# Performance work log

Hardware: AMD Instinct MI355X
Metric: run time of the kernel (lower is better)

The kernel has to match this reference:

```python
import jax, jax.numpy as jnp
import numpy as np

N, E, B = 25600, 307200, 256
H, D, F0, K = 256, 16, 7, 6
GNN_OUT, TDA_IN, TDA_OUT, MEG_IN, MEG_OUT = 192, 32, 128, 16, 64
FUSION = GNN_OUT + TDA_OUT + MEG_OUT  # 384
MID = FUSION // 2  # 192


def _ln(x, g, b, eps=1e-5):
    m = x.mean(-1, keepdims=True)
    v = x.var(-1, keepdims=True)
    return (x - m) * jax.lax.rsqrt(v + eps) * g + b


def _ntn(x, pos, neg):
    return jnp.nan_to_num(x, nan=0.0, posinf=pos, neginf=neg)


def setup_inputs():
    key = jax.random.key(0)
    ks = iter(jax.random.split(key, 80))
    p = lambda *s: 0.05 * jax.random.normal(next(ks), s, jnp.float32)
    inp = {
        "x": jax.random.normal(next(ks), (N, F0), jnp.float32),
        "edge_attr": jax.random.uniform(next(ks), (E, D), dtype=jnp.float32),
        "tda": jax.random.normal(next(ks), (B, TDA_IN), jnp.float32),
        "megnet": jax.random.normal(next(ks), (B, MEG_IN), jnp.float32),
        "edge_index": jax.random.randint(next(ks), (2, E), 0, N),
        "batch": jnp.repeat(jnp.arange(B), N // B),
        # GNN encoder
        "gin_W": p(F0, H), "gin_b": jnp.zeros(H),
        "conv_Wf": p(6, 2 * H + D, H), "conv_bf": jnp.zeros((6, H)),
        "conv_Ws": p(6, 2 * H + D, H), "conv_bs": jnp.zeros((6, H)),
        "gln_g": jnp.ones((6, H)), "gln_b": jnp.zeros((6, H)),
        "gout_W": p(H, GNN_OUT), "gout_b": jnp.zeros(GNN_OUT),
        # TDA projector 32->256->256->128
        "t1_W": p(TDA_IN, 2 * TDA_OUT), "t1_b": jnp.zeros(2 * TDA_OUT),
        "tln1_g": jnp.ones(2 * TDA_OUT), "tln1_b": jnp.zeros(2 * TDA_OUT),
        "t2_W": p(2 * TDA_OUT, 2 * TDA_OUT), "t2_b": jnp.zeros(2 * TDA_OUT),
        "tln2_g": jnp.ones(2 * TDA_OUT), "tln2_b": jnp.zeros(2 * TDA_OUT),
        "t3_W": p(2 * TDA_OUT, TDA_OUT), "t3_b": jnp.zeros(TDA_OUT),
        # MEGNet projector 16->128->128->64
        "m1_W": p(MEG_IN, 2 * MEG_OUT), "m1_b": jnp.zeros(2 * MEG_OUT),
        "mln1_g": jnp.ones(2 * MEG_OUT), "mln1_b": jnp.zeros(2 * MEG_OUT),
        "m2_W": p(2 * MEG_OUT, 2 * MEG_OUT), "m2_b": jnp.zeros(2 * MEG_OUT),
        "mln2_g": jnp.ones(2 * MEG_OUT), "mln2_b": jnp.zeros(2 * MEG_OUT),
        "m3_W": p(2 * MEG_OUT, MEG_OUT), "m3_b": jnp.zeros(MEG_OUT),
        # fusion LN
        "fln_g": jnp.ones(FUSION), "fln_b": jnp.zeros(FUSION),
        # CPPN gate 384->48->24->6
        "g1_W": p(FUSION, K * 8), "g1_b": jnp.zeros(K * 8),
        "hln_g": jnp.ones(K * 8), "hln_b": jnp.zeros(K * 8),
        "g2_W": p(K * 8, K * 4), "g2_b": jnp.zeros(K * 4),
        "g3_W": p(K * 4, K), "g3_b": jnp.zeros(K),
        # CPPN poly branches stacked over K
        "plin_W": p(K, FUSION), "plin_b": jnp.zeros(K),
        "pq1_W": p(K, FUSION, MID), "pq1_b": jnp.zeros((K, MID)),
        "pq2_W": p(K, MID), "pq2_b": jnp.zeros(K),
        "pc1_W": p(K, FUSION, MID // 2), "pc1_b": jnp.zeros((K, MID // 2)),
        "pc2_W": p(K, MID // 2), "pc2_b": jnp.zeros(K),
    }
    return inp


def _forward(x, edge_attr, tda, megnet, edge_index, batch,
             gin_W, gin_b, conv_Wf, conv_bf, conv_Ws, conv_bs, gln_g, gln_b, gout_W, gout_b,
             t1_W, t1_b, tln1_g, tln1_b, t2_W, t2_b, tln2_g, tln2_b, t3_W, t3_b,
             m1_W, m1_b, mln1_g, mln1_b, m2_W, m2_b, mln2_g, mln2_b, m3_W, m3_b,
             fln_g, fln_b,
             g1_W, g1_b, hln_g, hln_b, g2_W, g2_b, g3_W, g3_b,
             plin_W, plin_b, pq1_W, pq1_b, pq2_W, pq2_b, pc1_W, pc1_b, pc2_W, pc2_b):
    silu = jax.nn.silu
    tda = _ntn(tda, 3.0, -3.0)
    megnet = _ntn(megnet, 3.0, -3.0)
    x = _ntn(x, 3.0, -3.0)
    ea = _ntn(edge_attr, 1.0, 0.0)
    src, dst = edge_index[0], edge_index[1]

    h = silu(x @ gin_W + gin_b)  # [N, H]
    for i in range(6):
        # CGConv message: z_ij = [x_i, x_j, e_ij]; sigmoid(z Wf) * softplus(z Ws); sum-agg + root
        z = jnp.concatenate([h[dst], h[src], ea], axis=-1)  # [E, 2H+D]
        msg = jax.nn.sigmoid(z @ conv_Wf[i] + conv_bf[i]) * jax.nn.softplus(z @ conv_Ws[i] + conv_bs[i])
        conv = h + jax.ops.segment_sum(msg, dst, num_segments=N)
        h = _ln(silu(conv) + h, gln_g[i], gln_b[i])
    cnt = jax.ops.segment_sum(jnp.ones((N, 1), h.dtype), batch, num_segments=B)
    pooled = jax.ops.segment_sum(h, batch, num_segments=B) / jnp.maximum(cnt, 1.0)
    z_gnn = jnp.nan_to_num(pooled @ gout_W + gout_b)  # [B, 192]

    # --- projectors ---
    a = _ln(silu(tda @ t1_W + t1_b), tln1_g, tln1_b)
    a = _ln(silu(a @ t2_W + t2_b), tln2_g, tln2_b)
    z_tda = jnp.nan_to_num(a @ t3_W + t3_b)  # [B, 128]
    m = _ln(silu(megnet @ m1_W + m1_b), mln1_g, mln1_b)
    m = _ln(silu(m @ m2_W + m2_b), mln2_g, mln2_b)
    z_meg = jnp.nan_to_num(m @ m3_W + m3_b)  # [B, 64]

    z = _ln(jnp.concatenate([z_gnn, z_tda, z_meg], axis=-1), fln_g, fln_b)  # [B, 384]

    # --- CPPN mixture head ---
    g = _ln(silu(z @ g1_W + g1_b), hln_g, hln_b)
    g = silu(g @ g2_W + g2_b)
    gates = jax.nn.softmax(g @ g3_W + g3_b, axis=-1)  # [B, K]
    lin = jnp.einsum('bd,kd->bk', z, plin_W) + plin_b
    hq = silu(jnp.einsum('bd,kdm->bkm', z, pq1_W) + pq1_b)  # [B, K, 192]
    q = jnp.einsum('bkm,km->bk', hq, pq2_W) + pq2_b
    hc = silu(jnp.einsum('bd,kdm->bkm', z, pc1_W) + pc1_b) ** 2  # [B, K, 96]
    c = jnp.einsum('bkm,km->bk', hc, pc2_W) + pc2_b
    y = (gates * (lin + q + c)).sum(-1)  # [B]
    return y, z


def reference(x, edge_attr, tda, megnet, edge_index, batch,
              gin_W, gin_b, conv_Wf, conv_bf, conv_Ws, conv_bs, gln_g, gln_b, gout_W, gout_b,
              t1_W, t1_b, tln1_g, tln1_b, t2_W, t2_b, tln2_g, tln2_b, t3_W, t3_b,
              m1_W, m1_b, mln1_g, mln1_b, m2_W, m2_b, mln2_g, mln2_b, m3_W, m3_b,
              fln_g, fln_b,
              g1_W, g1_b, hln_g, hln_b, g2_W, g2_b, g3_W, g3_b,
              plin_W, plin_b, pq1_W, pq1_b, pq2_W, pq2_b, pc1_W, pc1_b, pc2_W, pc2_b):
    return _forward(x, edge_attr, tda, megnet, edge_index, batch,
                    gin_W, gin_b, conv_Wf, conv_bf, conv_Ws, conv_bs, gln_g, gln_b, gout_W, gout_b,
                    t1_W, t1_b, tln1_g, tln1_b, t2_W, t2_b, tln2_g, tln2_b, t3_W, t3_b,
                    m1_W, m1_b, mln1_g, mln1_b, m2_W, m2_b, mln2_g, mln2_b, m3_W, m3_b,
                    fln_g, fln_b,
                    g1_W, g1_b, hln_g, hln_b, g2_W, g2_b, g3_W, g3_b,
                    plin_W, plin_b, pq1_W, pq1_b, pq2_W, pq2_b, pc1_W, pc1_b, pc2_W, pc2_b)
```

## Files before the change

### kernel.cpp

```cpp
#include <hip/hip_runtime.h>
#include <hip/hip_bf16.h>
#include <cmath>

#define NN 25600
#define NE 307200
#define NB 256
#define HD 256

typedef __attribute__((ext_vector_type(8))) short short8;
typedef __attribute__((ext_vector_type(4))) float f32x4;
typedef __attribute__((ext_vector_type(2))) float f32x2;
typedef __attribute__((ext_vector_type(2))) _Float16 h16x2;
typedef __attribute__((ext_vector_type(2))) __fp16 fp16x2;

__device__ __forceinline__ float ntn_f(float v, float pos, float neg) {
  if (isnan(v)) return 0.f;
  if (isinf(v)) return v > 0.f ? pos : neg;
  return v;
}
__device__ __forceinline__ float ntn_def(float v) {
  if (isnan(v)) return 0.f;
  if (isinf(v)) return v > 0.f ? 3.4028234663852886e38f : -3.4028234663852886e38f;
  return v;
}
__device__ __forceinline__ float sigmoid_f(float x) { return 1.f / (1.f + __expf(-x)); }
__device__ __forceinline__ float silu_f(float x) { return x * sigmoid_f(x); }
__device__ __forceinline__ float softplus_f(float x) {
  return fmaxf(x, 0.f) + __logf(1.f + __expf(-fabsf(x)));
}
__device__ __forceinline__ unsigned short f2bf(float f) {
  unsigned int u = __float_as_uint(f);
  u += 0x7fffu + ((u >> 16) & 1u);
  return (unsigned short)(u >> 16);
}
__device__ __forceinline__ float bfu(unsigned short u) {
  return __uint_as_float((unsigned int)u << 16);
}
__device__ __forceinline__ h16x2 u2h(unsigned int u) {
  union { unsigned int u; h16x2 h; } x; x.u = u; return x.h;
}
__device__ __forceinline__ unsigned int pk2u(float a, float b) {
  union { fp16x2 p; unsigned int u; } x;
  x.p = __builtin_amdgcn_cvt_pkrtz(a, b);
  return x.u;
}
#if __has_builtin(__builtin_amdgcn_fdot2)
#define FDOT2(a, b, c) __builtin_amdgcn_fdot2((a), (b), (c), false)
#else
__device__ __forceinline__ float fdot2_sw(h16x2 a, h16x2 b, float c) {
  return (float)a.x * (float)b.x + (float)a.y * (float)b.y + c;
}
#define FDOT2(a, b, c) fdot2_sw((a), (b), (c))
#endif

template <int NW>
__device__ __forceinline__ float blockSum(float v, float* sred) {
  int lane = threadIdx.x & 63, w = threadIdx.x >> 6;
#pragma unroll
  for (int o = 32; o; o >>= 1) v += __shfl_xor(v, o);
  __syncthreads();
  if (lane == 0) sred[w] = v;
  __syncthreads();
  float r = 0.f;
#pragma unroll
  for (int i = 0; i < NW; ++i) r += sred[i];
  return r;
}

__global__ void k_hist(const int* __restrict__ dst, int* __restrict__ counts, int E) {
  int e = blockIdx.x * 256 + threadIdx.x;
  if (e < E) atomicAdd(&counts[dst[e]], 1);
}

__global__ __launch_bounds__(1024) void k_scan(const int* __restrict__ counts,
                                               int* __restrict__ offs, int n) {
  __shared__ int sd[1024];
  __shared__ int run;
  int tid = threadIdx.x;
  if (tid == 0) run = 0;
  __syncthreads();
  for (int base = 0; base < n; base += 1024) {
    int i = base + tid;
    int v = (i < n) ? counts[i] : 0;
    sd[tid] = v;
    __syncthreads();
    int acc = v;
    for (int off = 1; off < 1024; off <<= 1) {
      int t = (tid >= off) ? sd[tid - off] : 0;
      __syncthreads();
      acc += t;
      sd[tid] = acc;
      __syncthreads();
    }
    int r = run;
    if (i < n) offs[i] = r + acc - v;
    __syncthreads();
    if (tid == 1023) run = r + sd[1023];
    __syncthreads();
  }
  if (threadIdx.x == 0) offs[n] = run;
}

__global__ void k_scatter(const int* __restrict__ dst, const int* __restrict__ offs,
                          int* __restrict__ cursor, int* __restrict__ eidx, int E) {
  int e = blockIdx.x * 256 + threadIdx.x;
  if (e < E) {
    int d = dst[e];
    int p = offs[d] + atomicAdd(&cursor[d], 1);
    eidx[p] = e;
  }
}

__global__ void k_srcperm(const int* __restrict__ eidx, const int* __restrict__ srcArr,
                          int* __restrict__ srcs, int E) {
  int i = blockIdx.x * 256 + threadIdx.x;
  if (i < E) srcs[i] = srcArr[eidx[i]];
}

__global__ void k_eapermh(const int* __restrict__ eidx, const float* __restrict__ ea,
                          unsigned int* __restrict__ eah, int E) {
  int gid = blockIdx.x * 256 + threadIdx.x;
  if (gid < E * 8) {
    int ii = gid >> 3, kp = gid & 7;
    int e = eidx[ii];
    float v0 = ea[(size_t)e * 16 + 2 * kp];
    float v1 = ea[(size_t)e * 16 + 2 * kp + 1];
    eah[gid] = pk2u(v0, v1);
  }
}

__global__ void k_pack(const float* __restrict__ conv_Wf, const float* __restrict__ conv_Ws,
                       unsigned short* __restrict__ w4t) {
  int layer = blockIdx.y;
  int gid = blockIdx.x * 256 + threadIdx.x;
  int k = gid & 255;
  int c = gid >> 8;
  int j = c & 255;
  int tbl = c >> 8;
  const float* W = (tbl < 2) ? conv_Wf : conv_Ws;
  int krow = (tbl & 1) ? 256 + k : k;
  float v = W[((size_t)layer * 528 + krow) * 256 + j];
  w4t[((size_t)layer * 1024 + c) * 256 + k] = f2bf(v);
}

__global__ void k_packEd(const float* __restrict__ conv_Wf, const float* __restrict__ conv_Ws,
                         unsigned int* __restrict__ whd) {
  int layer = blockIdx.y;
  int gid = blockIdx.x * 256 + threadIdx.x;
  int d = gid >> 4, pr = gid & 15;
  int g = pr >> 3, kp = pr & 7;
  const float* W = g ? conv_Ws : conv_Wf;
  float v0 = W[((size_t)layer * 528 + 512 + 2 * kp) * 256 + d];
  float v1 = W[((size_t)layer * 528 + 512 + 2 * kp + 1) * 256 + d];
  whd[((size_t)layer * 256 + d) * 16 + pr] = pk2u(v0, v1);
}

__global__ void k_gin(const float* __restrict__ x, const float* __restrict__ W,
                      const float* __restrict__ bias, float* __restrict__ h,
                      unsigned short* __restrict__ hbf) {
  int n = blockIdx.x, j = threadIdx.x;
  float xv[7];
#pragma unroll
  for (int k = 0; k < 7; ++k) xv[k] = ntn_f(x[n * 7 + k], 3.f, -3.f);
  float acc = bias[j];
#pragma unroll
  for (int k = 0; k < 7; ++k) acc += xv[k] * W[k * 256 + j];
  float o = silu_f(acc);
  h[(size_t)n * 256 + j] = o;
  hbf[(size_t)n * 256 + j] = f2bf(o);
}

__global__ __launch_bounds__(256) void k_gemm_bf16(
    const unsigned short* __restrict__ Abf,
    const unsigned short* __restrict__ w4t,
    const float* __restrict__ bf, const float* __restrict__ bs,
    unsigned short* __restrict__ Pout) {
  __shared__ unsigned short As[128 * 56];
  __shared__ unsigned short Bs[128 * 56];
  int tid = threadIdx.x;
  int lane = tid & 63, w = tid >> 6;
  int wr = w >> 1, wc = w & 1;
  int m0 = blockIdx.x * 128, n0 = blockIdx.y * 128;
  int l15 = lane & 15, l4 = lane >> 4;
  f32x4 acc[4][4];
#pragma unroll
  for (int i = 0; i < 4; ++i)
#pragma unroll
    for (int j = 0; j < 4; ++j) acc[i][j] = (f32x4)0.f;
  for (int kt = 0; kt < 8; ++kt) {
    int k0 = kt * 32;
    if (kt) __syncthreads();
#pragma unroll
    for (int c = 0; c < 2; ++c) {
      int chunk = tid + c * 256;
      int row = chunk >> 2, q = chunk & 3;
      *(uint4*)&As[row * 56 + q * 8] =
          *(const uint4*)&Abf[(size_t)(m0 + row) * 256 + k0 + q * 8];
      *(uint4*)&Bs[row * 56 + q * 8] =
          *(const uint4*)&w4t[(size_t)(n0 + row) * 256 + k0 + q * 8];
    }
    __syncthreads();
    short8 a[4], b[4];
#pragma unroll
    for (int f = 0; f < 4; ++f) {
      a[f] = *(const short8*)&As[(wr * 64 + f * 16 + l15) * 56 + l4 * 8];
      b[f] = *(const short8*)&Bs[(wc * 64 + f * 16 + l15) * 56 + l4 * 8];
    }
#pragma unroll
    for (int i = 0; i < 4; ++i)
#pragma unroll
      for (int j = 0; j < 4; ++j)
        acc[i][j] = __builtin_amdgcn_mfma_f32_16x16x32_bf16(a[i], b[j], acc[i][j], 0, 0, 0);
  }
#pragma unroll
  for (int j = 0; j < 4; ++j) {
    int gcol = n0 + wc * 64 + j * 16 + l15;
    float bias = (gcol < 256) ? bf[gcol] : (gcol >= 512 && gcol < 768) ? bs[gcol - 512] : 0.f;
#pragma unroll
    for (int i = 0; i < 4; ++i) {
#pragma unroll
      for (int r = 0; r < 4; ++r) {
        int grow = m0 + wr * 64 + i * 16 + l4 * 4 + r;
        Pout[(size_t)grow * 1024 + gcol] = f2bf(acc[i][j][r] + bias);
      }
    }
  }
}

__global__ __launch_bounds__(256) void k_edge4(
    const float* __restrict__ h, const unsigned short* __restrict__ P,
    const unsigned int* __restrict__ eah,
    const int* __restrict__ srcs, const int* __restrict__ offs,
    const unsigned int* __restrict__ whd,
    const float* __restrict__ lng, const float* __restrict__ lnb,
    float* __restrict__ hout, unsigned short* __restrict__ hbfout) {
  __shared__ float sr1[4], sr2[4];
  int tid = threadIdx.x, lane = tid & 63, w = tid >> 6;
  int n = blockIdx.x;
  int d = w * 64 + lane;

  unsigned int wk[16];
  {
    const uint4* wb = (const uint4*)(whd + (size_t)d * 16);
#pragma unroll
    for (int q = 0; q < 4; ++q) {
      uint4 t = wb[q];
      wk[q * 4 + 0] = t.x; wk[q * 4 + 1] = t.y;
      wk[q * 4 + 2] = t.z; wk[q * 4 + 3] = t.w;
    }
  }
  float lg = lng[d], lb = lnb[d];
  const unsigned short* Pn = P + (size_t)n * 1024;
  float pfd = bfu(Pn[d]);
  float psd = bfu(Pn[512 + d]);
  float hn = h[(size_t)n * 256 + d];
  float acc = 0.f;
  int e0 = __builtin_amdgcn_readfirstlane(offs[n]);
  int e1 = __builtin_amdgcn_readfirstlane(offs[n + 1]);

  for (int ii = e0; ii < e1; ++ii) {
    int s = srcs[ii];
    const unsigned short* Ps = P + (size_t)s * 1024;
    unsigned short uf = Ps[256 + d];
    unsigned short us = Ps[768 + d];
    const uint4* e4 = (const uint4*)(eah + (size_t)ii * 8);
    uint4 ea0 = e4[0], ea1 = e4[1];
    unsigned int ec[8] = {ea0.x, ea0.y, ea0.z, ea0.w, ea1.x, ea1.y, ea1.z, ea1.w};
    float af = pfd, as_ = psd;
#pragma unroll
    for (int kp = 0; kp < 8; ++kp) {
      h16x2 c = u2h(ec[kp]);
      af = FDOT2(u2h(wk[kp]), c, af);
      as_ = FDOT2(u2h(wk[8 + kp]), c, as_);
    }
    af += bfu(uf);
    as_ += bfu(us);
    acc += sigmoid_f(af) * softplus_f(as_);
  }
  float cv = hn + acc;
  float t = silu_f(cv) + hn;
  float s1 = t, s2 = t * t;
#pragma unroll
  for (int o = 32; o; o >>= 1) {
    s1 += __shfl_xor(s1, o);
    s2 += __shfl_xor(s2, o);
  }
  if (lane == 0) { sr1[w] = s1; sr2[w] = s2; }
  __syncthreads();
  float S1 = sr1[0] + sr1[1] + sr1[2] + sr1[3];
  float S2 = sr2[0] + sr2[1] + sr2[2] + sr2[3];
  float mean = S1 * (1.f / 256.f);
  float var = S2 * (1.f / 256.f) - mean * mean;
  float inv = rsqrtf(var + 1e-5f);
  float o0 = (t - mean) * inv * lg + lb;
  hout[(size_t)n * 256 + d] = o0;
  hbfout[(size_t)n * 256 + d] = f2bf(o0);
}

__global__ __launch_bounds__(256) void k_pool2(const float* __restrict__ h,
                                               float* __restrict__ pooled) {
  int b = blockIdx.x, j = threadIdx.x;
  const float* hp = h + (size_t)b * 100 * 256 + j;
  float s = 0.f;
  for (int i = 0; i < 100; ++i) s += hp[(size_t)i * 256];
  pooled[b * 256 + j] = s * 0.01f;
}

__global__ void k_zgnn(const float* __restrict__ pooled,
                       const float* __restrict__ W, const float* __restrict__ bias,
                       float* __restrict__ zf) {
  int b = blockIdx.x, j = threadIdx.x;
  float acc = bias[j];
  for (int k = 0; k < 256; ++k) acc += pooled[b * 256 + k] * W[k * 192 + j];
  zf[b * 384 + j] = ntn_def(acc);
}

__global__ __launch_bounds__(256) void k_tda(const float* __restrict__ tda,
    const float* __restrict__ W1, const float* __restrict__ b1,
    const float* __restrict__ g1, const float* __restrict__ bb1,
    const float* __restrict__ W2, const float* __restrict__ b2,
    const float* __restrict__ g2, const float* __restrict__ bb2,
    const float* __restrict__ W3, const float* __restrict__ b3, float* __restrict__ zf) {
  __shared__ float sin_[32];
  __shared__ float sa[256];
  __shared__ float sred[4];
  int b = blockIdx.x, tid = threadIdx.x;
  if (tid < 32) sin_[tid] = ntn_f(tda[b * 32 + tid], 3.f, -3.f);
  __syncthreads();
  float v = b1[tid];
#pragma unroll
  for (int k = 0; k < 32; ++k) v += sin_[k] * W1[k * 256 + tid];
  v = silu_f(v);
  float s1 = blockSum<4>(v, sred);
  float s2 = blockSum<4>(v * v, sred);
  float mean = s1 * (1.f / 256.f), var = s2 * (1.f / 256.f) - mean * mean;
  float inv = rsqrtf(var + 1e-5f);
  v = (v - mean) * inv * g1[tid] + bb1[tid];
  sa[tid] = v;
  __syncthreads();
  float v2 = b2[tid];
  for (int k = 0; k < 256; ++k) v2 += sa[k] * W2[k * 256 + tid];
  v2 = silu_f(v2);
  s1 = blockSum<4>(v2, sred);
  s2 = blockSum<4>(v2 * v2, sred);
  mean = s1 * (1.f / 256.f); var = s2 * (1.f / 256.f) - mean * mean;
  inv = rsqrtf(var + 1e-5f);
  v2 = (v2 - mean) * inv * g2[tid] + bb2[tid];
  __syncthreads();
  sa[tid] = v2;
  __syncthreads();
  if (tid < 128) {
    float o = b3[tid];
    for (int k = 0; k < 256; ++k) o += sa[k] * W3[k * 128 + tid];
    zf[b * 384 + 192 + tid] = ntn_def(o);
  }
}

__global__ __launch_bounds__(128) void k_meg(const float* __restrict__ mg,
    const float* __restrict__ W1, const float* __restrict__ b1,
    const float* __restrict__ g1, const float* __restrict__ bb1,
    const float* __restrict__ W2, const float* __restrict__ b2,
    const float* __restrict__ g2, const float* __restrict__ bb2,
    const float* __restrict__ W3, const float* __restrict__ b3, float* __restrict__ zf) {
  __shared__ float sin_[16];
  __shared__ float sa[128];
  __shared__ float sred[2];
  int b = blockIdx.x, tid = threadIdx.x;
  if (tid < 16) sin_[tid] = ntn_f(mg[b * 16 + tid], 3.f, -3.f);
  __syncthreads();
  float v = b1[tid];
#pragma unroll
  for (int k = 0; k < 16; ++k) v += sin_[k] * W1[k * 128 + tid];
  v = silu_f(v);
  float s1 = blockSum<2>(v, sred);
  float s2 = blockSum<2>(v * v, sred);
  float mean = s1 * (1.f / 128.f), var = s2 * (1.f / 128.f) - mean * mean;
  float inv = rsqrtf(var + 1e-5f);
  v = (v - mean) * inv * g1[tid] + bb1[tid];
  sa[tid] = v;
  __syncthreads();
  float v2 = b2[tid];
  for (int k = 0; k < 128; ++k) v2 += sa[k] * W2[k * 128 + tid];
  v2 = silu_f(v2);
  s1 = blockSum<2>(v2, sred);
  s2 = blockSum<2>(v2 * v2, sred);
  mean = s1 * (1.f / 128.f); var = s2 * (1.f / 128.f) - mean * mean;
  inv = rsqrtf(var + 1e-5f);
  v2 = (v2 - mean) * inv * g2[tid] + bb2[tid];
  __syncthreads();
  sa[tid] = v2;
  __syncthreads();
  if (tid < 64) {
    float o = b3[tid];
    for (int k = 0; k < 128; ++k) o += sa[k] * W3[k * 64 + tid];
    zf[b * 384 + 320 + tid] = ntn_def(o);
  }
}

__global__ __launch_bounds__(384) void k_cppn(const float* __restrict__ zf,
    const float* __restrict__ flng, const float* __restrict__ flnb,
    const float* __restrict__ g1W, const float* __restrict__ g1b,
    const float* __restrict__ hg, const float* __restrict__ hb,
    const float* __restrict__ g2W, const float* __restrict__ g2b,
    const float* __restrict__ g3W, const float* __restrict__ g3b,
    const float* __restrict__ plW, const float* __restrict__ plb,
    const float* __restrict__ pq1W, const float* __restrict__ pq1b,
    const float* __restrict__ pq2W, const float* __restrict__ pq2b,
    const float* __restrict__ pc1W, const float* __restrict__ pc1b,
    const float* __restrict__ pc2W, const float* __restrict__ pc2b,
    float* __restrict__ zout, float* __restrict__ y) {
  __shared__ float sz[384];
  __shared__ float sred[6];
  __shared__ float sg[48];
  __shared__ float s24[24];
  __shared__ float gates[6];
  __shared__ float lin[6];
  __shared__ float qv[6], cvv[6];
  __shared__ float mn48, iv48;
  __shared__ float prodq[1152];
  __shared__ float prodc[576];
  int b = blockIdx.x, tid = threadIdx.x;
  int lane = tid & 63, wv = tid >> 6;

  float v = zf[(size_t)b * 384 + tid];
  float s1 = blockSum<6>(v, sred);
  float s2 = blockSum<6>(v * v, sred);
  float mean = s1 * (1.f / 384.f), var = s2 * (1.f / 384.f) - mean * mean;
  float inv = rsqrtf(var + 1e-5f);
  float zv = (v - mean) * inv * flng[tid] + flnb[tid];
  sz[tid] = zv;
  zout[(size_t)b * 384 + tid] = zv;
  __syncthreads();

  {
    int j = tid >> 3, p = tid & 7;
    float a = 0.f;
    for (int d = p; d < 384; d += 8) a += sz[d] * g1W[d * 48 + j];
    a += __shfl_xor(a, 1);
    a += __shfl_xor(a, 2);
    a += __shfl_xor(a, 4);
    if (p == 0) sg[j] = silu_f(a + g1b[j]);
  }
  __syncthreads();
  if (tid < 64) {
    float x = (tid < 48) ? sg[tid] : 0.f;
    float t1 = x, t2 = x * x;
#pragma unroll
    for (int o = 32; o; o >>= 1) {
      t1 += __shfl_xor(t1, o);
      t2 += __shfl_xor(t2, o);
    }
    if (tid == 0) {
      mn48 = t1 * (1.f / 48.f);
      float vr = t2 * (1.f / 48.f) - mn48 * mn48;
      iv48 = rsqrtf(vr + 1e-5f);
    }
  }
  __syncthreads();
  if (tid < 48) sg[tid] = (sg[tid] - mn48) * iv48 * hg[tid] + hb[tid];
  __syncthreads();
  {
    int j = tid >> 4, p = tid & 15;
    int d0 = p * 3;
    float a = sg[d0] * g2W[d0 * 24 + j] + sg[d0 + 1] * g2W[(d0 + 1) * 24 + j] +
              sg[d0 + 2] * g2W[(d0 + 2) * 24 + j];
    a += __shfl_xor(a, 1);
    a += __shfl_xor(a, 2);
    a += __shfl_xor(a, 4);
    a += __shfl_xor(a, 8);
    if (p == 0) s24[j] = silu_f(a + g2b[j]);
  }
  __syncthreads();
  if (tid < 6) {
    float a = g3b[tid];
    for (int k = 0; k < 24; ++k) a += s24[k] * g3W[k * 6 + tid];
    gates[tid] = a;
  }
  __syncthreads();
  if (tid == 0) {
    float mx = gates[0];
    for (int i = 1; i < 6; ++i) mx = fmaxf(mx, gates[i]);
    float s = 0.f;
    for (int i = 0; i < 6; ++i) { gates[i] = __expf(gates[i] - mx); s += gates[i]; }
    float rs = 1.f / s;
    for (int i = 0; i < 6; ++i) gates[i] *= rs;
  }
  {
    float p = 0.f;
    for (int d = lane; d < 384; d += 64) p += sz[d] * plW[wv * 384 + d];
#pragma unroll
    for (int o = 32; o; o >>= 1) p += __shfl_xor(p, o);
    if (lane == 0) lin[wv] = p + plb[wv];
  }
  if (tid < 288) {
    int k = tid / 48, m4 = (tid % 48) * 4;
    f32x4 a = (f32x4)0.f;
    const float* Wp = pq1W + (size_t)k * 384 * 192 + m4;
    for (int d = 0; d < 384; ++d) {
      float4 w4 = *(const float4*)(Wp + (size_t)d * 192);
      float zd = sz[d];
      a.x += zd * w4.x; a.y += zd * w4.y; a.z += zd * w4.z; a.w += zd * w4.w;
    }
#pragma unroll
    for (int r = 0; r < 4; ++r) {
      int m = m4 + r;
      prodq[k * 192 + m] = silu_f(a[r] + pq1b[k * 192 + m]) * pq2W[k * 192 + m];
    }
  }
  if (tid < 144) {
    int k = tid / 24, m4 = (tid % 24) * 4;
    f32x4 a = (f32x4)0.f;
    const float* Wp = pc1W + (size_t)k * 384 * 96 + m4;
    for (int d = 0; d < 384; ++d) {
      float4 w4 = *(const float4*)(Wp + (size_t)d * 96);
      float zd = sz[d];
      a.x += zd * w4.x; a.y += zd * w4.y; a.z += zd * w4.z; a.w += zd * w4.w;
    }
#pragma unroll
    for (int r = 0; r < 4; ++r) {
      int m = m4 + r;
      float sl = silu_f(a[r] + pc1b[k * 96 + m]);
      prodc[k * 96 + m] = sl * sl * pc2W[k * 96 + m];
    }
  }
  __syncthreads();
  {
    float s = prodq[wv * 192 + lane] + prodq[wv * 192 + 64 + lane] +
              prodq[wv * 192 + 128 + lane];
#pragma unroll
    for (int o = 32; o; o >>= 1) s += __shfl_xor(s, o);
    if (lane == 0) qv[wv] = s + pq2b[wv];
    float c = prodc[wv * 96 + lane];
    float c2 = (lane < 32) ? prodc[wv * 96 + 64 + lane] : 0.f;
    float sc = c + c2;
#pragma unroll
    for (int o = 32; o; o >>= 1) sc += __shfl_xor(sc, o);
    if (lane == 0) cvv[wv] = sc + pc2b[wv];
  }
  __syncthreads();
  if (tid == 0) {
    float yy = 0.f;
    for (int k = 0; k < 6; ++k) yy += gates[k] * (lin[k] + qv[k] + cvv[k]);
    y[b] = yy;
  }
}

extern "C" void kernel_launch(void* const* d_in, const int* in_sizes, int n_in,
                              void* d_out, int out_size, void* d_ws, size_t ws_size,
                              hipStream_t stream) {
  const float* x         = (const float*)d_in[0];
  const float* edge_attr = (const float*)d_in[1];
  const float* tda       = (const float*)d_in[2];
  const float* megnet    = (const float*)d_in[3];
  const int*   edge_index= (const int*)d_in[4];
  const float* gin_W = (const float*)d_in[6];
  const float* gin_b = (const float*)d_in[7];
  const float* conv_Wf = (const float*)d_in[8];
  const float* conv_bf = (const float*)d_in[9];
  const float* conv_Ws = (const float*)d_in[10];
  const float* conv_bs = (const float*)d_in[11];
  const float* gln_g = (const float*)d_in[12];
  const float* gln_b = (const float*)d_in[13];
  const float* gout_W = (const float*)d_in[14];
  const float* gout_b = (const float*)d_in[15];
  const float* t1_W = (const float*)d_in[16];
  const float* t1_b = (const float*)d_in[17];
  const float* tln1_g = (const float*)d_in[18];
  const float* tln1_b = (const float*)d_in[19];
  const float* t2_W = (const float*)d_in[20];
  const float* t2_b = (const float*)d_in[21];
  const float* tln2_g = (const float*)d_in[22];
  const float* tln2_b = (const float*)d_in[23];
  const float* t3_W = (const float*)d_in[24];
  const float* t3_b = (const float*)d_in[25];
  const float* m1_W = (const float*)d_in[26];
  const float* m1_b = (const float*)d_in[27];
  const float* mln1_g = (const float*)d_in[28];
  const float* mln1_b = (const float*)d_in[29];
  const float* m2_W = (const float*)d_in[30];
  const float* m2_b = (const float*)d_in[31];
  const float* mln2_g = (const float*)d_in[32];
  const float* mln2_b = (const float*)d_in[33];
  const float* m3_W = (const float*)d_in[34];
  const float* m3_b = (const float*)d_in[35];
  const float* fln_g = (const float*)d_in[36];
  const float* fln_b = (const float*)d_in[37];
  const float* g1_W = (const float*)d_in[38];
  const float* g1_b = (const float*)d_in[39];
  const float* hln_g = (const float*)d_in[40];
  const float* hln_b = (const float*)d_in[41];
  const float* g2_W = (const float*)d_in[42];
  const float* g2_b = (const float*)d_in[43];
  const float* g3_W = (const float*)d_in[44];
  const float* g3_b = (const float*)d_in[45];
  const float* plin_W = (const float*)d_in[46];
  const float* plin_b = (const float*)d_in[47];
  const float* pq1_W = (const float*)d_in[48];
  const float* pq1_b = (const float*)d_in[49];
  const float* pq2_W = (const float*)d_in[50];
  const float* pq2_b = (const float*)d_in[51];
  const float* pc1_W = (const float*)d_in[52];
  const float* pc1_b = (const float*)d_in[53];
  const float* pc2_W = (const float*)d_in[54];
  const float* pc2_b = (const float*)d_in[55];

  float* ws = (float*)d_ws;
  float* hA = ws;
  float* hB = hA + (size_t)NN * 256;
  float* pooled = hB + (size_t)NN * 256;
  float* zf = pooled + (size_t)NB * 256;
  unsigned short* hbfA = (unsigned short*)(zf + (size_t)NB * 384);
  unsigned short* hbfB = hbfA + (size_t)NN * 256;
  unsigned short* Pbf = hbfB + (size_t)NN * 256;
  unsigned short* w4t = Pbf + (size_t)NN * 1024;
  unsigned int* whd6 = (unsigned int*)(w4t + (size_t)6 * 1024 * 256);
  unsigned int* eah = whd6 + (size_t)6 * 256 * 16;
  int* counts = (int*)(eah + (size_t)NE * 8);
  int* cursor = counts + NN;
  int* offs = cursor + NN;
  int* eidx = offs + NN + 1;
  int* srcs = eidx + NE;

  const int* srcArr = edge_index;
  const int* dstArr = edge_index + NE;

  hipMemsetAsync(counts, 0, (size_t)2 * NN * sizeof(int), stream);

  k_hist<<<(NE + 255) / 256, 256, 0, stream>>>(dstArr, counts, NE);
  k_scan<<<1, 1024, 0, stream>>>(counts, offs, NN);
  k_scatter<<<(NE + 255) / 256, 256, 0, stream>>>(dstArr, offs, cursor, eidx, NE);
  k_srcperm<<<(NE + 255) / 256, 256, 0, stream>>>(eidx, srcArr, srcs, NE);
  k_eapermh<<<(NE * 8 + 255) / 256, 256, 0, stream>>>(eidx, edge_attr, eah, NE);
  k_pack<<<dim3(1024, 6), 256, 0, stream>>>(conv_Wf, conv_Ws, w4t);
  k_packEd<<<dim3(16, 6), 256, 0, stream>>>(conv_Wf, conv_Ws, whd6);

  k_gin<<<NN, 256, 0, stream>>>(x, gin_W, gin_b, hA, hbfA);

  float* hcur = hA;          float* hnext = hB;
  unsigned short* bcur = hbfA; unsigned short* bnext = hbfB;
  for (int i = 0; i < 6; ++i) {
    k_gemm_bf16<<<dim3(NN / 128, 8), 256, 0, stream>>>(
        bcur, w4t + (size_t)i * 1024 * 256, conv_bf + i * 256, conv_bs + i * 256, Pbf);
    k_edge4<<<NN, 256, 0, stream>>>(hcur, Pbf, eah, srcs, offs,
                                    whd6 + (size_t)i * 256 * 16,
                                    gln_g + i * 256, gln_b + i * 256, hnext, bnext);
    float* tf = hcur; hcur = hnext; hnext = tf;
    unsigned short* tb = bcur; bcur = bnext; bnext = tb;
  }

  k_pool2<<<NB, 256, 0, stream>>>(hcur, pooled);
  k_zgnn<<<NB, 192, 0, stream>>>(pooled, gout_W, gout_b, zf);
  k_tda<<<NB, 256, 0, stream>>>(tda, t1_W, t1_b, tln1_g, tln1_b, t2_W, t2_b, tln2_g, tln2_b,
                                t3_W, t3_b, zf);
  k_meg<<<NB, 128, 0, stream>>>(megnet, m1_W, m1_b, mln1_g, mln1_b, m2_W, m2_b, mln2_g, mln2_b,
                                m3_W, m3_b, zf);

  float* yout = (float*)d_out;
  float* zout = yout + NB;
  k_cppn<<<NB, 384, 0, stream>>>(zf, fln_g, fln_b,
                                 g1_W, g1_b, hln_g, hln_b, g2_W, g2_b, g3_W, g3_b,
                                 plin_W, plin_b, pq1_W, pq1_b, pq2_W, pq2_b,
                                 pc1_W, pc1_b, pc2_W, pc2_b, zout, yout);
}
```

Before: 1.199 ms.

## Switch edge-attribute projection from fp16 dot2 to fp32 FMA with LDS weights

The edge kernel now computes the 16-wide edge-attribute projection in fp32 FMAs instead of packed fp16 dot2 instructions. The edge attributes are permuted into CSR order as fp32, and each block stages the 32x256 fp32 weight slice in shared memory instead of holding packed fp16 weights in registers. This removes fp16 rounding and frees 16 VGPRs. In exchange it doubles edge-attribute traffic, adds per-block LDS fills of 32 KB plus a barrier for 25600 blocks, and doubles the ALU op count in the inner loop. The 32 KB of LDS per block may also limit occupancy.

Result: slower. 1.710 ms (+42.6%).

```diff
diff --git a/kernel.cpp b/kernel.cpp
--- a/kernel.cpp
+++ b/kernel.cpp
@@ -10,8 +10,6 @@
 typedef __attribute__((ext_vector_type(8))) short short8;
 typedef __attribute__((ext_vector_type(4))) float f32x4;
 typedef __attribute__((ext_vector_type(2))) float f32x2;
-typedef __attribute__((ext_vector_type(2))) _Float16 h16x2;
-typedef __attribute__((ext_vector_type(2))) __fp16 fp16x2;
 
 __device__ __forceinline__ float ntn_f(float v, float pos, float neg) {
   if (isnan(v)) return 0.f;
@@ -36,22 +34,6 @@
 __device__ __forceinline__ float bfu(unsigned short u) {
   return __uint_as_float((unsigned int)u << 16);
 }
-__device__ __forceinline__ h16x2 u2h(unsigned int u) {
-  union { unsigned int u; h16x2 h; } x; x.u = u; return x.h;
-}
-__device__ __forceinline__ unsigned int pk2u(float a, float b) {
-  union { fp16x2 p; unsigned int u; } x;
-  x.p = __builtin_amdgcn_cvt_pkrtz(a, b);
-  return x.u;
-}
-#if __has_builtin(__builtin_amdgcn_fdot2)
-#define FDOT2(a, b, c) __builtin_amdgcn_fdot2((a), (b), (c), false)
-#else
-__device__ __forceinline__ float fdot2_sw(h16x2 a, h16x2 b, float c) {
-  return (float)a.x * (float)b.x + (float)a.y * (float)b.y + c;
-}
-#define FDOT2(a, b, c) fdot2_sw((a), (b), (c))
-#endif
 
 template <int NW>
 __device__ __forceinline__ float blockSum(float v, float* sred) {
@@ -117,15 +99,12 @@
   if (i < E) srcs[i] = srcArr[eidx[i]];
 }
 
-__global__ void k_eapermh(const int* __restrict__ eidx, const float* __restrict__ ea,
-                          unsigned int* __restrict__ eah, int E) {
+__global__ void k_eaperm(const int* __restrict__ eidx, const float* __restrict__ ea,
+                         float* __restrict__ eacsr, int E) {
   int gid = blockIdx.x * 256 + threadIdx.x;
-  if (gid < E * 8) {
-    int ii = gid >> 3, kp = gid & 7;
-    int e = eidx[ii];
-    float v0 = ea[(size_t)e * 16 + 2 * kp];
-    float v1 = ea[(size_t)e * 16 + 2 * kp + 1];
-    eah[gid] = pk2u(v0, v1);
+  if (gid < E * 16) {
+    int ii = gid >> 4, k = gid & 15;
+    eacsr[gid] = ea[(size_t)eidx[ii] * 16 + k];
   }
 }
 
@@ -143,16 +122,14 @@
   w4t[((size_t)layer * 1024 + c) * 256 + k] = f2bf(v);
 }
 
-__global__ void k_packEd(const float* __restrict__ conv_Wf, const float* __restrict__ conv_Ws,
-                         unsigned int* __restrict__ whd) {
+__global__ void k_packEf(const float* __restrict__ conv_Wf, const float* __restrict__ conv_Ws,
+                         float* __restrict__ wf32) {
   int layer = blockIdx.y;
   int gid = blockIdx.x * 256 + threadIdx.x;
-  int d = gid >> 4, pr = gid & 15;
-  int g = pr >> 3, kp = pr & 7;
+  int pr = gid >> 8, d = gid & 255;
+  int g = pr >> 4, k = pr & 15;
   const float* W = g ? conv_Ws : conv_Wf;
-  float v0 = W[((size_t)layer * 528 + 512 + 2 * kp) * 256 + d];
-  float v1 = W[((size_t)layer * 528 + 512 + 2 * kp + 1) * 256 + d];
-  whd[((size_t)layer * 256 + d) * 16 + pr] = pk2u(v0, v1);
+  wf32[((size_t)layer * 32 + pr) * 256 + d] = W[((size_t)layer * 528 + 512 + k) * 256 + d];
 }
 
 __global__ void k_gin(const float* __restrict__ x, const float* __restrict__ W,
@@ -227,28 +204,27 @@
   }
 }
 
-__global__ __launch_bounds__(256) void k_edge4(
+__global__ __launch_bounds__(256) void k_edge6(
     const float* __restrict__ h, const unsigned short* __restrict__ P,
-    const unsigned int* __restrict__ eah,
+    const float* __restrict__ eacsr,
     const int* __restrict__ srcs, const int* __restrict__ offs,
-    const unsigned int* __restrict__ whd,
+    const float* __restrict__ wf32,
     const float* __restrict__ lng, const float* __restrict__ lnb,
     float* __restrict__ hout, unsigned short* __restrict__ hbfout) {
+  __shared__ float wldsf[32 * 256];
   __shared__ float sr1[4], sr2[4];
   int tid = threadIdx.x, lane = tid & 63, w = tid >> 6;
   int n = blockIdx.x;
   int d = w * 64 + lane;
 
-  unsigned int wk[16];
   {
-    const uint4* wb = (const uint4*)(whd + (size_t)d * 16);
-#pragma unroll
-    for (int q = 0; q < 4; ++q) {
-      uint4 t = wb[q];
-      wk[q * 4 + 0] = t.x; wk[q * 4 + 1] = t.y;
-      wk[q * 4 + 2] = t.z; wk[q * 4 + 3] = t.w;
-    }
-  }
+    const float4* g = (const float4*)wf32;
+    float4* l = (float4*)wldsf;
+#pragma unroll
+    for (int q = 0; q < 8; ++q) l[q * 256 + tid] = g[q * 256 + tid];
+  }
+  __syncthreads();
+
   float lg = lng[d], lb = lnb[d];
   const unsigned short* Pn = P + (size_t)n * 1024;
   float pfd = bfu(Pn[d]);
@@ -257,21 +233,20 @@
   float acc = 0.f;
   int e0 = __builtin_amdgcn_readfirstlane(offs[n]);
   int e1 = __builtin_amdgcn_readfirstlane(offs[n + 1]);
+  const unsigned short* Pf = P + 256 + d;
 
   for (int ii = e0; ii < e1; ++ii) {
     int s = srcs[ii];
-    const unsigned short* Ps = P + (size_t)s * 1024;
-    unsigned short uf = Ps[256 + d];
-    unsigned short us = Ps[768 + d];
-    const uint4* e4 = (const uint4*)(eah + (size_t)ii * 8);
-    uint4 ea0 = e4[0], ea1 = e4[1];
-    unsigned int ec[8] = {ea0.x, ea0.y, ea0.z, ea0.w, ea1.x, ea1.y, ea1.z, ea1.w};
+    size_t so = (size_t)s * 1024;
+    unsigned short uf = Pf[so];
+    unsigned short us = Pf[so + 512];
+    const float* eaP = eacsr + ((size_t)ii << 4);
     float af = pfd, as_ = psd;
 #pragma unroll
-    for (int kp = 0; kp < 8; ++kp) {
-      h16x2 c = u2h(ec[kp]);
-      af = FDOT2(u2h(wk[kp]), c, af);
-      as_ = FDOT2(u2h(wk[8 + kp]), c, as_);
+    for (int k = 0; k < 16; ++k) {
+      float c = eaP[k];
+      af = fmaf(c, wldsf[k * 256 + d], af);
+      as_ = fmaf(c, wldsf[(16 + k) * 256 + d], as_);
     }
     af += bfu(uf);
     as_ += bfu(us);
@@ -609,13 +584,13 @@
   float* hB = hA + (size_t)NN * 256;
   float* pooled = hB + (size_t)NN * 256;
   float* zf = pooled + (size_t)NB * 256;
-  unsigned short* hbfA = (unsigned short*)(zf + (size_t)NB * 384);
+  float* eacsr = zf + (size_t)NB * 384;
+  float* wf32 = eacsr + (size_t)NE * 16;
+  unsigned short* hbfA = (unsigned short*)(wf32 + (size_t)6 * 32 * 256);
   unsigned short* hbfB = hbfA + (size_t)NN * 256;
   unsigned short* Pbf = hbfB + (size_t)NN * 256;
   unsigned short* w4t = Pbf + (size_t)NN * 1024;
-  unsigned int* whd6 = (unsigned int*)(w4t + (size_t)6 * 1024 * 256);
-  unsigned int* eah = whd6 + (size_t)6 * 256 * 16;
-  int* counts = (int*)(eah + (size_t)NE * 8);
+  int* counts = (int*)(w4t + (size_t)6 * 1024 * 256);
   int* cursor = counts + NN;
   int* offs = cursor + NN;
   int* eidx = offs + NN + 1;
@@ -630,9 +605,9 @@
   k_scan<<<1, 1024, 0, stream>>>(counts, offs, NN);
   k_scatter<<<(NE + 255) / 256, 256, 0, stream>>>(dstArr, offs, cursor, eidx, NE);
   k_srcperm<<<(NE + 255) / 256, 256, 0, stream>>>(eidx, srcArr, srcs, NE);
-  k_eapermh<<<(NE * 8 + 255) / 256, 256, 0, stream>>>(eidx, edge_attr, eah, NE);
+  k_eaperm<<<(NE * 16 + 255) / 256, 256, 0, stream>>>(eidx, edge_attr, eacsr, NE);
   k_pack<<<dim3(1024, 6), 256, 0, stream>>>(conv_Wf, conv_Ws, w4t);
-  k_packEd<<<dim3(16, 6), 256, 0, stream>>>(conv_Wf, conv_Ws, whd6);
+  k_packEf<<<dim3(32, 6), 256, 0, stream>>>(conv_Wf, conv_Ws, wf32);
 
   k_gin<<<NN, 256, 0, stream>>>(x, gin_W, gin_b, hA, hbfA);
 
@@ -641,8 +616,8 @@
   for (int i = 0; i < 6; ++i) {
     k_gemm_bf16<<<dim3(NN / 128, 8), 256, 0, stream>>>(
         bcur, w4t + (size_t)i * 1024 * 256, conv_bf + i * 256, conv_bs + i * 256, Pbf);
-    k_edge4<<<NN, 256, 0, stream>>>(hcur, Pbf, eah, srcs, offs,
-                                    whd6 + (size_t)i * 256 * 16,
+    k_edge6<<<NN, 256, 0, stream>>>(hcur, Pbf, eacsr, srcs, offs,
+                                    wf32 + (size_t)i * 32 * 256,
                                     gln_g + i * 256, gln_b + i * 256, hnext, bnext);
     float* tf = hcur; hcur = hnext; hnext = tf;
     unsigned short* tb = bcur; bcur = bnext; bnext = tb;
```
